# Performance work log

Measured on AMD Instinct MI355X. Metric: run time of the kernel, lower is better.

## Reference

```python
import jax, jax.numpy as jnp
import numpy as np

C, NHEAD, WIN = 192, 6, 8

def setup_inputs() -> dict:
    key = jax.random.key(0)
    ks = jax.random.split(key, 16)
    B, H, W = 4, 256, 256
    s = 0.02
    inp = {
        "q2d": jax.random.normal(ks[0], (B, C, H, W), jnp.float32),
        "kv2d": jax.random.normal(ks[1], (B, C, H, W), jnp.float32),
        "wq": jax.random.normal(ks[2], (C, C), jnp.float32) * s,
        "bq": jnp.zeros((C,), jnp.float32),
        "wk": jax.random.normal(ks[3], (C, C), jnp.float32) * s,
        "bk": jnp.zeros((C,), jnp.float32),
        "wv": jax.random.normal(ks[4], (C, C), jnp.float32) * s,
        "bv": jnp.zeros((C,), jnp.float32),
        "in_w": jax.random.normal(ks[5], (3 * C, C), jnp.float32) * s,
        "in_b": jnp.zeros((3 * C,), jnp.float32),
        "out_w": jax.random.normal(ks[6], (C, C), jnp.float32) * s,
        "out_b": jnp.zeros((C,), jnp.float32),
        "proj_w": jax.random.normal(ks[7], (C, C), jnp.float32) * s,
        "proj_b": jnp.zeros((C,), jnp.float32),
    }
    return inp

def _conv1x1(x, w, b):
    # x: [B,C,H,W], w: [O,C] (1x1 conv kernel), b: [O]
    return jnp.einsum('bchw,oc->bohw', x, w) + b[None, :, None, None]

def reference(q2d, kv2d, wq, bq, wk, bk, wv, bv, in_w, in_b, out_w, out_b, proj_w, proj_b):
    B, c, H, W = q2d.shape
    w = WIN
    Hb, Wb = H // w, W // w  # H,W chosen divisible by window -> pad is a no-op
    L = Hb * Wb
    S = w * w
    hd = c // NHEAD

    q = _conv1x1(q2d, wq, bq)
    k = _conv1x1(kv2d, wk, bk)
    v = _conv1x1(kv2d, wv, bv)

    def to_seq(t):
        # unfold(kernel=w, stride=w) -> blocks row-major over (Hb, Wb), tokens row-major within window
        return t.reshape(B, c, Hb, w, Wb, w).transpose(0, 2, 4, 3, 5, 1).reshape(B * L, S, c)

    qs, ks_, vs = to_seq(q), to_seq(k), to_seq(v)

    # nn.MultiheadAttention internal projections
    wq_i, wk_i, wv_i = jnp.split(in_w, 3, axis=0)
    bq_i, bk_i, bv_i = jnp.split(in_b, 3, axis=0)

    def heads(t, wgt, b):
        return (t @ wgt.T + b).reshape(B * L, S, NHEAD, hd).transpose(0, 2, 1, 3)

    qh = heads(qs, wq_i, bq_i)
    kh = heads(ks_, wk_i, bk_i)
    vh = heads(vs, wv_i, bv_i)

    scores = jnp.einsum('nhsd,nhtd->nhst', qh, kh) / jnp.sqrt(jnp.float32(hd))
    attn = jax.nn.softmax(scores, axis=-1)
    o = jnp.einsum('nhst,nhtd->nhsd', attn, vh)
    o = o.transpose(0, 2, 1, 3).reshape(B * L, S, c) @ out_w.T + out_b

    # fold back: [B*L, S, C] -> [B, C, H, W]
    o2d = o.reshape(B, Hb, Wb, w, w, c).transpose(0, 5, 1, 3, 2, 4).reshape(B, c, H, W)
    out = _conv1x1(o2d, proj_w, proj_b)
    return out + q2d
```

## Files before the change

### kernel.cpp

```cpp
#include <hip/hip_runtime.h>

#define CC 192
#define WFRAG_USHORTS (4*6*12*512)
#define SX 202

typedef __attribute__((ext_vector_type(8))) short bf16x8;
typedef __attribute__((ext_vector_type(4))) float f32x4;

__device__ __forceinline__ unsigned short f2b(float f){
  unsigned u = __float_as_uint(f);
  return (unsigned short)((u + 0x7fffu + ((u >> 16) & 1u)) >> 16);
}
__device__ __forceinline__ unsigned pk2(float a, float b){
  return (unsigned)f2b(a) | ((unsigned)f2b(b) << 16);
}

__global__ void fuse_weights(const float* __restrict__ wq, const float* __restrict__ bq,
                             const float* __restrict__ wk, const float* __restrict__ bk,
                             const float* __restrict__ wv, const float* __restrict__ bv,
                             const float* __restrict__ in_w, const float* __restrict__ in_b,
                             const float* __restrict__ out_w, const float* __restrict__ out_b,
                             const float* __restrict__ proj_w, const float* __restrict__ proj_b,
                             unsigned short* __restrict__ Wf, float* __restrict__ Bf)
{
  int mat = blockIdx.x / CC, o = blockIdx.x % CC, ci = threadIdx.x;
  const float *A, *Bm, *bs, *ba; int aoff, boff; float scale = 1.f;
  if (mat == 0){ A=in_w; aoff=0;    Bm=wq;    bs=bq;    ba=in_b;   boff=0;    scale=0.17677669529663687f; }
  else if (mat==1){ A=in_w; aoff=CC;   Bm=wk;    bs=bk;    ba=in_b;   boff=CC;   }
  else if (mat==2){ A=in_w; aoff=2*CC; Bm=wv;    bs=bv;    ba=in_b;   boff=2*CC; }
  else            { A=proj_w; aoff=0;  Bm=out_w; bs=out_b; ba=proj_b; boff=0;    }
  const float* ar = A + (size_t)(aoff + o) * CC;
  float acc = 0.f;
  for (int m = 0; m < CC; ++m) acc = fmaf(ar[m], Bm[m*CC + ci], acc);
  int k = ci >> 5, n = o >> 4, lgv = (ci >> 3) & 3, e = ci & 7;
  int lane = (o & 15) | (lgv << 4);
  Wf[(((mat*6 + k)*12 + n) << 9) + lane*8 + e] = f2b(acc * scale);
  if (ci == 0){
    float bacc = 0.f;
    for (int m = 0; m < CC; ++m) bacc = fmaf(ar[m], bs[m], bacc);
    Bf[mat*CC + o] = (bacc + ba[boff + o]) * scale;
  }
}

__global__ __launch_bounds__(256, 2) void win_attn(
    const float* __restrict__ q2d, const float* __restrict__ kv2d,
    const unsigned short* __restrict__ Wf, const float* __restrict__ Bf,
    float* __restrict__ out)
{
  __shared__ unsigned short B1[64*SX];
  __shared__ unsigned short B2[64*SX];
  __shared__ unsigned short VT[192*72];

  const int t = threadIdx.x;
  const int w = t >> 6, lane = t & 63, lr = lane & 15, lg = lane >> 4;
  const int bid = blockIdx.x;
  const int wid = (bid & 7) * 512 + (bid >> 3);
  const int b = wid >> 10, l = wid & 1023;
  const int y0 = (l >> 5) << 3, x0 = (l & 31) << 3;
  const float* qsrc  = q2d  + (size_t)b * CC * 65536;
  const float* kvsrc = kv2d + (size_t)b * CC * 65536;
  const int n0 = w * 3;

  auto stage = [&](const float* __restrict__ src, unsigned short* __restrict__ dst){
    #pragma unroll
    for (int i = 0; i < 6; ++i){
      int lin = i*256 + t;
      int c2 = lin >> 4, tok0 = (lin & 15) << 2;
      int gy = (y0 + (tok0 >> 3)) * 256 + x0 + (tok0 & 7);
      float4 va = *(const float4*)&src[(size_t)(2*c2)   * 65536 + gy];
      float4 vb = *(const float4*)&src[(size_t)(2*c2+1) * 65536 + gy];
      float fa[4] = {va.x, va.y, va.z, va.w};
      float fb[4] = {vb.x, vb.y, vb.z, vb.w};
      #pragma unroll
      for (int j = 0; j < 4; ++j)
        *(unsigned*)&dst[(tok0 + j)*SX + 2*c2] = pk2(fa[j], fb[j]);
    }
  };

  stage(qsrc, B1);
  stage(kvsrc, B2);
  __syncthreads();

  auto projAcc = [&](const unsigned short* __restrict__ Xs, int mat, f32x4 (&acc)[3][4]){
    #pragma unroll
    for (int k = 0; k < 6; ++k){
      bf16x8 a[4];
      #pragma unroll
      for (int m = 0; m < 4; ++m)
        a[m] = *(const bf16x8*)&Xs[(m*16 + lr)*SX + k*32 + lg*8];
      #pragma unroll
      for (int u = 0; u < 3; ++u){
        bf16x8 bw = *(const bf16x8*)&Wf[(((mat*6 + k)*12 + n0 + u) << 9) + lane*8];
        #pragma unroll
        for (int m = 0; m < 4; ++m)
          acc[u][m] = __builtin_amdgcn_mfma_f32_16x16x32_bf16(a[m], bw, acc[u][m], 0, 0, 0);
      }
    }
  };

  f32x4 qacc[3][4] = {};
  projAcc(B1, 0, qacc);
  {
    f32x4 vacc[3][4] = {};
    projAcc(B2, 2, vacc);
    #pragma unroll
    for (int u = 0; u < 3; ++u){
      int row = (n0 + u)*16 + lr;
      float bb = Bf[2*CC + row];
      #pragma unroll
      for (int m = 0; m < 4; ++m){
        *(unsigned*)&VT[row*72 + m*16 + lg*4]     = pk2(vacc[u][m][0] + bb, vacc[u][m][1] + bb);
        *(unsigned*)&VT[row*72 + m*16 + lg*4 + 2] = pk2(vacc[u][m][2] + bb, vacc[u][m][3] + bb);
      }
    }
  }
  f32x4 kacc[3][4] = {};
  projAcc(B2, 1, kacc);
  __syncthreads();

  #pragma unroll
  for (int u = 0; u < 3; ++u){
    int ch = (n0 + u)*16 + lr;
    float bq_ = Bf[0*CC + ch], bk_ = Bf[1*CC + ch];
    #pragma unroll
    for (int m = 0; m < 4; ++m)
      #pragma unroll
      for (int rr = 0; rr < 4; ++rr){
        B1[(m*16 + lg*4 + rr)*SX + ch] = f2b(qacc[u][m][rr] + bq_);
        B2[(m*16 + lg*4 + rr)*SX + ch] = f2b(kacc[u][m][rr] + bk_);
      }
  }
  __syncthreads();

  {
    const int r0 = w * 16;
    #pragma unroll
    for (int h = 0; h < 6; ++h){
      f32x4 st[4] = {};
      bf16x8 bq_ = *(const bf16x8*)&B1[(r0 + lr)*SX + h*32 + lg*8];
      #pragma unroll
      for (int m = 0; m < 4; ++m){
        bf16x8 a = *(const bf16x8*)&B2[(m*16 + lr)*SX + h*32 + lg*8];
        st[m] = __builtin_amdgcn_mfma_f32_16x16x32_bf16(a, bq_, st[m], 0, 0, 0);
      }
      float mx = st[0][0];
      #pragma unroll
      for (int m = 0; m < 4; ++m)
        #pragma unroll
        for (int rr = 0; rr < 4; ++rr) mx = fmaxf(mx, st[m][rr]);
      mx = fmaxf(mx, __shfl_xor(mx, 16));
      mx = fmaxf(mx, __shfl_xor(mx, 32));
      float p[16]; float s = 0.f;
      #pragma unroll
      for (int m = 0; m < 4; ++m)
        #pragma unroll
        for (int rr = 0; rr < 4; ++rr){ float e = __expf(st[m][rr] - mx); p[m*4+rr] = e; s += e; }
      s += __shfl_xor(s, 16); s += __shfl_xor(s, 32);
      float inv = 1.f / s;
      #pragma unroll
      for (int i2 = 0; i2 < 16; ++i2) p[i2] *= inv;
      f32x4 o0 = {}, o1 = {};
      #pragma unroll
      for (int kt = 0; kt < 2; ++kt){
        bf16x8 ap;
        ((unsigned*)&ap)[0] = pk2(p[8*kt+0], p[8*kt+1]);
        ((unsigned*)&ap)[1] = pk2(p[8*kt+2], p[8*kt+3]);
        ((unsigned*)&ap)[2] = pk2(p[8*kt+4], p[8*kt+5]);
        ((unsigned*)&ap)[3] = pk2(p[8*kt+6], p[8*kt+7]);
        bf16x8 v0, v1;
        ((uint2*)&v0)[0] = *(const uint2*)&VT[(h*32 + lr)*72      + kt*32 + lg*4];
        ((uint2*)&v0)[1] = *(const uint2*)&VT[(h*32 + lr)*72      + kt*32 + 16 + lg*4];
        ((uint2*)&v1)[0] = *(const uint2*)&VT[(h*32 + 16 + lr)*72 + kt*32 + lg*4];
        ((uint2*)&v1)[1] = *(const uint2*)&VT[(h*32 + 16 + lr)*72 + kt*32 + 16 + lg*4];
        o0 = __builtin_amdgcn_mfma_f32_16x16x32_bf16(ap, v0, o0, 0, 0, 0);
        o1 = __builtin_amdgcn_mfma_f32_16x16x32_bf16(ap, v1, o1, 0, 0, 0);
      }
      #pragma unroll
      for (int rr = 0; rr < 4; ++rr){
        int tok = r0 + lg*4 + rr;
        B1[tok*SX + h*32 + lr]      = f2b(o0[rr]);
        B1[tok*SX + h*32 + 16 + lr] = f2b(o1[rr]);
      }
    }
  }
  __syncthreads();

  {
    f32x4 eo[3][4] = {};
    #pragma unroll
    for (int k = 0; k < 6; ++k){
      bf16x8 bo[4];
      #pragma unroll
      for (int nt = 0; nt < 4; ++nt)
        bo[nt] = *(const bf16x8*)&B1[(nt*16 + lr)*SX + k*32 + lg*8];
      #pragma unroll
      for (int u = 0; u < 3; ++u){
        bf16x8 aw = *(const bf16x8*)&Wf[(((18 + k)*12 + n0 + u) << 9) + lane*8];
        #pragma unroll
        for (int nt = 0; nt < 4; ++nt)
          eo[u][nt] = __builtin_amdgcn_mfma_f32_16x16x32_bf16(aw, bo[nt], eo[u][nt], 0, 0, 0);
      }
    }
    #pragma unroll
    for (int u = 0; u < 3; ++u){
      #pragma unroll
      for (int rr = 0; rr < 4; ++rr){
        int o = (n0 + u)*16 + lg*4 + rr;
        float bb = Bf[3*CC + o];
        #pragma unroll
        for (int nt = 0; nt < 4; ++nt){
          int tok = nt*16 + lr;
          size_t g = (size_t)(b*CC + o)*65536 + (size_t)(y0 + (tok >> 3))*256 + x0 + (tok & 7);
          out[g] = eo[u][nt][rr] + bb + q2d[g];
        }
      }
    }
  }
}

extern "C" void kernel_launch(void* const* d_in, const int* in_sizes, int n_in,
                              void* d_out, int out_size, void* d_ws, size_t ws_size,
                              hipStream_t stream)
{
  const float* q2d    = (const float*)d_in[0];
  const float* kv2d   = (const float*)d_in[1];
  const float* wq     = (const float*)d_in[2];
  const float* bq     = (const float*)d_in[3];
  const float* wk     = (const float*)d_in[4];
  const float* bk     = (const float*)d_in[5];
  const float* wv     = (const float*)d_in[6];
  const float* bv     = (const float*)d_in[7];
  const float* in_w   = (const float*)d_in[8];
  const float* in_b   = (const float*)d_in[9];
  const float* out_w  = (const float*)d_in[10];
  const float* out_b  = (const float*)d_in[11];
  const float* proj_w = (const float*)d_in[12];
  const float* proj_b = (const float*)d_in[13];

  unsigned short* Wf = (unsigned short*)d_ws;
  float* Bf = (float*)((char*)d_ws + WFRAG_USHORTS*2);
  float* out = (float*)d_out;

  fuse_weights<<<4*CC, CC, 0, stream>>>(wq,bq,wk,bk,wv,bv,in_w,in_b,
                                        out_w,out_b,proj_w,proj_b, Wf, Bf);
  win_attn<<<4096, 256, 0, stream>>>(q2d, kv2d, Wf, Bf, out);
}
```

Baseline: 328.6 us.

## Use 512-thread blocks and split Q/K/V projection work across eight waves

Doubles the block to eight waves per window. Waves 0-3 project Q and waves 4-7 project K, and each wave also computes half of the V token rows, so the Q/K/V projections run concurrently instead of as three serial passes. Attention tasks (head × 16-row tile) and the output projection are redistributed across the eight waves, and the VT stride changes to 74 to reduce LDS bank conflicts. This cuts per-wave serial MFMA work and register pressure, at the cost of larger blocks and occupancy that is now bounded by LDS use.

```diff
diff --git a/kernel.cpp b/kernel.cpp
--- a/kernel.cpp
+++ b/kernel.cpp
@@ -3,6 +3,7 @@
 #define CC 192
 #define WFRAG_USHORTS (4*6*12*512)
 #define SX 202
+#define SV 74
 
 typedef __attribute__((ext_vector_type(8))) short bf16x8;
 typedef __attribute__((ext_vector_type(4))) float f32x4;
@@ -42,14 +43,13 @@
   }
 }
 
-__global__ __launch_bounds__(256, 2) void win_attn(
+__global__ __launch_bounds__(512, 4) void win_attn(
     const float* __restrict__ q2d, const float* __restrict__ kv2d,
     const unsigned short* __restrict__ Wf, const float* __restrict__ Bf,
     float* __restrict__ out)
 {
-  __shared__ unsigned short B1[64*SX];
-  __shared__ unsigned short B2[64*SX];
-  __shared__ unsigned short VT[192*72];
+  __shared__ unsigned short QK[2][64*SX];
+  __shared__ unsigned short VT[192*SV];
 
   const int t = threadIdx.x;
   const int w = t >> 6, lane = t & 63, lr = lane & 15, lg = lane >> 4;
@@ -59,12 +59,14 @@
   const int y0 = (l >> 5) << 3, x0 = (l & 31) << 3;
   const float* qsrc  = q2d  + (size_t)b * CC * 65536;
   const float* kvsrc = kv2d + (size_t)b * CC * 65536;
-  const int n0 = w * 3;
+
+  const int mat = w >> 2;
+  const int tb  = 3 * (w & 3);
 
   auto stage = [&](const float* __restrict__ src, unsigned short* __restrict__ dst){
     #pragma unroll
-    for (int i = 0; i < 6; ++i){
-      int lin = i*256 + t;
+    for (int i = 0; i < 3; ++i){
+      int lin = i*512 + t;
       int c2 = lin >> 4, tok0 = (lin & 15) << 2;
       int gy = (y0 + (tok0 >> 3)) * 256 + x0 + (tok0 & 7);
       float4 va = *(const float4*)&src[(size_t)(2*c2)   * 65536 + gy];
@@ -77,141 +79,142 @@
     }
   };
 
-  stage(qsrc, B1);
-  stage(kvsrc, B2);
-  __syncthreads();
-
-  auto projAcc = [&](const unsigned short* __restrict__ Xs, int mat, f32x4 (&acc)[3][4]){
-    #pragma unroll
-    for (int k = 0; k < 6; ++k){
-      bf16x8 a[4];
+  stage(qsrc,  QK[0]);
+  stage(kvsrc, QK[1]);
+  __syncthreads();
+
+  const unsigned short* Xs = QK[mat];
+  f32x4 qk[3][4] = {};
+  f32x4 vv[3][2] = {};
+  #pragma unroll
+  for (int k = 0; k < 6; ++k){
+    bf16x8 a[4];
+    #pragma unroll
+    for (int m = 0; m < 4; ++m)
+      a[m] = *(const bf16x8*)&Xs[(m*16 + lr)*SX + k*32 + lg*8];
+    bf16x8 av[2];
+    #pragma unroll
+    for (int mi = 0; mi < 2; ++mi)
+      av[mi] = *(const bf16x8*)&QK[1][((2*mat + mi)*16 + lr)*SX + k*32 + lg*8];
+    #pragma unroll
+    for (int i = 0; i < 3; ++i){
+      bf16x8 bw = *(const bf16x8*)&Wf[(((mat*6 + k)*12 + tb + i) << 9) + lane*8];
       #pragma unroll
       for (int m = 0; m < 4; ++m)
-        a[m] = *(const bf16x8*)&Xs[(m*16 + lr)*SX + k*32 + lg*8];
-      #pragma unroll
-      for (int u = 0; u < 3; ++u){
-        bf16x8 bw = *(const bf16x8*)&Wf[(((mat*6 + k)*12 + n0 + u) << 9) + lane*8];
-        #pragma unroll
-        for (int m = 0; m < 4; ++m)
-          acc[u][m] = __builtin_amdgcn_mfma_f32_16x16x32_bf16(a[m], bw, acc[u][m], 0, 0, 0);
-      }
-    }
-  };
-
-  f32x4 qacc[3][4] = {};
-  projAcc(B1, 0, qacc);
+        qk[i][m] = __builtin_amdgcn_mfma_f32_16x16x32_bf16(a[m], bw, qk[i][m], 0, 0, 0);
+      bf16x8 bv = *(const bf16x8*)&Wf[(((12 + k)*12 + tb + i) << 9) + lane*8];
+      #pragma unroll
+      for (int mi = 0; mi < 2; ++mi)
+        vv[i][mi] = __builtin_amdgcn_mfma_f32_16x16x32_bf16(av[mi], bv, vv[i][mi], 0, 0, 0);
+    }
+  }
+  #pragma unroll
+  for (int i = 0; i < 3; ++i){
+    int ch = (tb + i)*16 + lr;
+    float bb = Bf[2*CC + ch];
+    #pragma unroll
+    for (int mi = 0; mi < 2; ++mi){
+      int tk = (2*mat + mi)*16 + lg*4;
+      *(unsigned*)&VT[ch*SV + tk]     = pk2(vv[i][mi][0] + bb, vv[i][mi][1] + bb);
+      *(unsigned*)&VT[ch*SV + tk + 2] = pk2(vv[i][mi][2] + bb, vv[i][mi][3] + bb);
+    }
+  }
+  __syncthreads();
+
   {
-    f32x4 vacc[3][4] = {};
-    projAcc(B2, 2, vacc);
-    #pragma unroll
-    for (int u = 0; u < 3; ++u){
-      int row = (n0 + u)*16 + lr;
-      float bb = Bf[2*CC + row];
-      #pragma unroll
-      for (int m = 0; m < 4; ++m){
-        *(unsigned*)&VT[row*72 + m*16 + lg*4]     = pk2(vacc[u][m][0] + bb, vacc[u][m][1] + bb);
-        *(unsigned*)&VT[row*72 + m*16 + lg*4 + 2] = pk2(vacc[u][m][2] + bb, vacc[u][m][3] + bb);
-      }
-    }
-  }
-  f32x4 kacc[3][4] = {};
-  projAcc(B2, 1, kacc);
-  __syncthreads();
-
-  #pragma unroll
-  for (int u = 0; u < 3; ++u){
-    int ch = (n0 + u)*16 + lr;
-    float bq_ = Bf[0*CC + ch], bk_ = Bf[1*CC + ch];
-    #pragma unroll
-    for (int m = 0; m < 4; ++m)
-      #pragma unroll
-      for (int rr = 0; rr < 4; ++rr){
-        B1[(m*16 + lg*4 + rr)*SX + ch] = f2b(qacc[u][m][rr] + bq_);
-        B2[(m*16 + lg*4 + rr)*SX + ch] = f2b(kacc[u][m][rr] + bk_);
-      }
-  }
-  __syncthreads();
-
-  {
-    const int r0 = w * 16;
-    #pragma unroll
-    for (int h = 0; h < 6; ++h){
-      f32x4 st[4] = {};
-      bf16x8 bq_ = *(const bf16x8*)&B1[(r0 + lr)*SX + h*32 + lg*8];
-      #pragma unroll
-      for (int m = 0; m < 4; ++m){
-        bf16x8 a = *(const bf16x8*)&B2[(m*16 + lr)*SX + h*32 + lg*8];
-        st[m] = __builtin_amdgcn_mfma_f32_16x16x32_bf16(a, bq_, st[m], 0, 0, 0);
-      }
-      float mx = st[0][0];
+    unsigned short* dst = QK[mat];
+    #pragma unroll
+    for (int i = 0; i < 3; ++i){
+      int ch = (tb + i)*16 + lr;
+      float bb = Bf[mat*CC + ch];
       #pragma unroll
       for (int m = 0; m < 4; ++m)
         #pragma unroll
-        for (int rr = 0; rr < 4; ++rr) mx = fmaxf(mx, st[m][rr]);
-      mx = fmaxf(mx, __shfl_xor(mx, 16));
-      mx = fmaxf(mx, __shfl_xor(mx, 32));
-      float p[16]; float s = 0.f;
-      #pragma unroll
-      for (int m = 0; m < 4; ++m)
+        for (int rr = 0; rr < 4; ++rr)
+          dst[(m*16 + lg*4 + rr)*SX + ch] = f2b(qk[i][m][rr] + bb);
+    }
+  }
+  __syncthreads();
+
+  #pragma unroll
+  for (int i = 0; i < 3; ++i){
+    int task = 3*w + i;
+    int h = task >> 2, r0 = (task & 3) << 4;
+    f32x4 st[4] = {};
+    bf16x8 bq_ = *(const bf16x8*)&QK[0][(r0 + lr)*SX + h*32 + lg*8];
+    #pragma unroll
+    for (int m = 0; m < 4; ++m){
+      bf16x8 a = *(const bf16x8*)&QK[1][(m*16 + lr)*SX + h*32 + lg*8];
+      st[m] = __builtin_amdgcn_mfma_f32_16x16x32_bf16(a, bq_, st[m], 0, 0, 0);
+    }
+    float mx = st[0][0];
+    #pragma unroll
+    for (int m = 0; m < 4; ++m)
+      #pragma unroll
+      for (int rr = 0; rr < 4; ++rr) mx = fmaxf(mx, st[m][rr]);
+    mx = fmaxf(mx, __shfl_xor(mx, 16));
+    mx = fmaxf(mx, __shfl_xor(mx, 32));
+    float p[16]; float s = 0.f;
+    #pragma unroll
+    for (int m = 0; m < 4; ++m)
+      #pragma unroll
+      for (int rr = 0; rr < 4; ++rr){ float e = __expf(st[m][rr] - mx); p[m*4+rr] = e; s += e; }
+    s += __shfl_xor(s, 16); s += __shfl_xor(s, 32);
+    float inv = 1.f / s;
+    #pragma unroll
+    for (int i2 = 0; i2 < 16; ++i2) p[i2] *= inv;
+    f32x4 o0 = {}, o1 = {};
+    #pragma unroll
+    for (int kt = 0; kt < 2; ++kt){
+      bf16x8 ap;
+      ((unsigned*)&ap)[0] = pk2(p[8*kt+0], p[8*kt+1]);
+      ((unsigned*)&ap)[1] = pk2(p[8*kt+2], p[8*kt+3]);
+      ((unsigned*)&ap)[2] = pk2(p[8*kt+4], p[8*kt+5]);
+      ((unsigned*)&ap)[3] = pk2(p[8*kt+6], p[8*kt+7]);
+      bf16x8 v0, v1;
+      ((uint2*)&v0)[0] = *(const uint2*)&VT[(h*32 + lr)*SV      + kt*32 + lg*4];
+      ((uint2*)&v0)[1] = *(const uint2*)&VT[(h*32 + lr)*SV      + kt*32 + 16 + lg*4];
+      ((uint2*)&v1)[0] = *(const uint2*)&VT[(h*32 + 16 + lr)*SV + kt*32 + lg*4];
+      ((uint2*)&v1)[1] = *(const uint2*)&VT[(h*32 + 16 + lr)*SV + kt*32 + 16 + lg*4];
+      o0 = __builtin_amdgcn_mfma_f32_16x16x32_bf16(ap, v0, o0, 0, 0, 0);
+      o1 = __builtin_amdgcn_mfma_f32_16x16x32_bf16(ap, v1, o1, 0, 0, 0);
+    }
+    #pragma unroll
+    for (int rr = 0; rr < 4; ++rr){
+      int tok = r0 + lg*4 + rr;
+      QK[0][tok*SX + h*32 + lr]      = f2b(o0[rr]);
+      QK[0][tok*SX + h*32 + 16 + lr] = f2b(o1[rr]);
+    }
+  }
+  __syncthreads();
+
+  {
+    f32x4 eo[3][2] = {};
+    #pragma unroll
+    for (int k = 0; k < 6; ++k){
+      bf16x8 bo[2];
+      #pragma unroll
+      for (int nt = 0; nt < 2; ++nt)
+        bo[nt] = *(const bf16x8*)&QK[0][((2*mat + nt)*16 + lr)*SX + k*32 + lg*8];
+      #pragma unroll
+      for (int i = 0; i < 3; ++i){
+        bf16x8 aw = *(const bf16x8*)&Wf[(((18 + k)*12 + tb + i) << 9) + lane*8];
         #pragma unroll
-        for (int rr = 0; rr < 4; ++rr){ float e = __expf(st[m][rr] - mx); p[m*4+rr] = e; s += e; }
-      s += __shfl_xor(s, 16); s += __shfl_xor(s, 32);
-      float inv = 1.f / s;
-      #pragma unroll
-      for (int i2 = 0; i2 < 16; ++i2) p[i2] *= inv;
-      f32x4 o0 = {}, o1 = {};
-      #pragma unroll
-      for (int kt = 0; kt < 2; ++kt){
-        bf16x8 ap;
-        ((unsigned*)&ap)[0] = pk2(p[8*kt+0], p[8*kt+1]);
-        ((unsigned*)&ap)[1] = pk2(p[8*kt+2], p[8*kt+3]);
-        ((unsigned*)&ap)[2] = pk2(p[8*kt+4], p[8*kt+5]);
-        ((unsigned*)&ap)[3] = pk2(p[8*kt+6], p[8*kt+7]);
-        bf16x8 v0, v1;
-        ((uint2*)&v0)[0] = *(const uint2*)&VT[(h*32 + lr)*72      + kt*32 + lg*4];
-        ((uint2*)&v0)[1] = *(const uint2*)&VT[(h*32 + lr)*72      + kt*32 + 16 + lg*4];
-        ((uint2*)&v1)[0] = *(const uint2*)&VT[(h*32 + 16 + lr)*72 + kt*32 + lg*4];
-        ((uint2*)&v1)[1] = *(const uint2*)&VT[(h*32 + 16 + lr)*72 + kt*32 + 16 + lg*4];
-        o0 = __builtin_amdgcn_mfma_f32_16x16x32_bf16(ap, v0, o0, 0, 0, 0);
-        o1 = __builtin_amdgcn_mfma_f32_16x16x32_bf16(ap, v1, o1, 0, 0, 0);
+        for (int nt = 0; nt < 2; ++nt)
+          eo[i][nt] = __builtin_amdgcn_mfma_f32_16x16x32_bf16(aw, bo[nt], eo[i][nt], 0, 0, 0);
       }
+    }
+    #pragma unroll
+    for (int i = 0; i < 3; ++i){
       #pragma unroll
       for (int rr = 0; rr < 4; ++rr){
-        int tok = r0 + lg*4 + rr;
-        B1[tok*SX + h*32 + lr]      = f2b(o0[rr]);
-        B1[tok*SX + h*32 + 16 + lr] = f2b(o1[rr]);
-      }
-    }
-  }
-  __syncthreads();
-
-  {
-    f32x4 eo[3][4] = {};
-    #pragma unroll
-    for (int k = 0; k < 6; ++k){
-      bf16x8 bo[4];
-      #pragma unroll
-      for (int nt = 0; nt < 4; ++nt)
-        bo[nt] = *(const bf16x8*)&B1[(nt*16 + lr)*SX + k*32 + lg*8];
-      #pragma unroll
-      for (int u = 0; u < 3; ++u){
-        bf16x8 aw = *(const bf16x8*)&Wf[(((18 + k)*12 + n0 + u) << 9) + lane*8];
-        #pragma unroll
-        for (int nt = 0; nt < 4; ++nt)
-          eo[u][nt] = __builtin_amdgcn_mfma_f32_16x16x32_bf16(aw, bo[nt], eo[u][nt], 0, 0, 0);
-      }
-    }
-    #pragma unroll
-    for (int u = 0; u < 3; ++u){
-      #pragma unroll
-      for (int rr = 0; rr < 4; ++rr){
-        int o = (n0 + u)*16 + lg*4 + rr;
+        int o = (tb + i)*16 + lg*4 + rr;
         float bb = Bf[3*CC + o];
         #pragma unroll
-        for (int nt = 0; nt < 4; ++nt){
-          int tok = nt*16 + lr;
+        for (int nt = 0; nt < 2; ++nt){
+          int tok = (2*mat + nt)*16 + lr;
           size_t g = (size_t)(b*CC + o)*65536 + (size_t)(y0 + (tok >> 3))*256 + x0 + (tok & 7);
-          out[g] = eo[u][nt][rr] + bb + q2d[g];
+          out[g] = eo[i][nt][rr] + bb + q2d[g];
         }
       }
     }
@@ -243,5 +246,5 @@
 
   fuse_weights<<<4*CC, CC, 0, stream>>>(wq,bq,wk,bk,wv,bv,in_w,in_b,
                                         out_w,out_b,proj_w,proj_b, Wf, Bf);
-  win_attn<<<4096, 256, 0, stream>>>(q2d, kv2d, Wf, Bf, out);
-}
+  win_attn<<<4096, 512, 0, stream>>>(q2d, kv2d, Wf, Bf, out);
+}
```

New measurement: 347.0 us. 1.06x slower.
